# Kernel tuning notes

Hardware: AMD Instinct MI355X
Metric: run time of the kernel (lower is better)

The kernel has to match this reference:

```python
import jax, jax.numpy as jnp
import numpy as np

B, S, DM, H = 4, 4096, 1024, 16
HD = DM // H

def setup_inputs() -> dict:
    key = jax.random.key(0)
    ks = jax.random.split(key, 9)
    sc = 1.0 / np.sqrt(DM)
    return {
        "x": jax.random.normal(ks[0], (B, S, DM), dtype=jnp.float32),
        "Wq": jax.random.normal(ks[1], (DM, DM), dtype=jnp.float32) * sc,
        "bq": jnp.zeros((DM,), dtype=jnp.float32),
        "Wk": jax.random.normal(ks[2], (DM, DM), dtype=jnp.float32) * sc,
        "bk": jnp.zeros((DM,), dtype=jnp.float32),
        "Wv": jax.random.normal(ks[3], (DM, DM), dtype=jnp.float32) * sc,
        "bv": jnp.zeros((DM,), dtype=jnp.float32),
        "Wo": jax.random.normal(ks[4], (DM, DM), dtype=jnp.float32) * sc,
        "bo": jnp.zeros((DM,), dtype=jnp.float32),
    }

def _heads(t):
    # [B,S,DM] -> [B,H,S,HD]
    return t.reshape(B, S, H, HD).transpose(0, 2, 1, 3)

def reference(x, Wq, bq, Wk, bk, Wv, bv, Wo, bo):
    q = _heads(x @ Wq.T + bq)
    k = _heads(x @ Wk.T + bk)
    v = _heads(x @ Wv.T + bv)
    q = jax.nn.elu(q) + 1.0  # positive feature map
    k = jax.nn.elu(k) + 1.0
    # kv aggregation: [B,H,HD,HD]
    kv = jnp.einsum('bhsd,bhse->bhde', k, v)
    qkv = jnp.einsum('bhsd,bhde->bhse', q, kv)  # [B,H,S,HD]
    k_sum = k.sum(axis=2)  # [B,H,HD]
    normalizer = jnp.einsum('bhsd,bhd->bhs', q, k_sum) + 1e-6
    out = qkv / normalizer[..., None]
    out = out.transpose(0, 2, 1, 3).reshape(B, S, DM)
    return out @ Wo.T + bo  # dropout is identity in eval
```

## Files before the change

### kernel.cpp

```cpp
#include <hip/hip_runtime.h>
#include <math.h>

#define NROWS  16384
#define DMODEL 1024
#define NHEAD  16
#define HDIM   64
#define SEQ    4096
#define NBATCH 4
#define NBH    64
#define SCHUNK 16
#define M1     1048576u

typedef __attribute__((ext_vector_type(8))) short bf16x8;
typedef __attribute__((ext_vector_type(4))) float f32x4;

#define VMCNT(N) asm volatile("s_waitcnt vmcnt(" #N ")" ::: "memory")
#define BAR() do { asm volatile("" ::: "memory"); __builtin_amdgcn_s_barrier(); \
                   asm volatile("" ::: "memory"); } while (0)

__device__ __forceinline__ unsigned short f2bf(float f) {
    unsigned u = __float_as_uint(f);
    u += 0x7FFFu + ((u >> 16) & 1u);
    return (unsigned short)(u >> 16);
}
__device__ __forceinline__ float bf2f(unsigned short h) {
    return __uint_as_float((unsigned)h << 16);
}

__device__ __forceinline__ void gload16(const void* g, void* l) {
    __builtin_amdgcn_global_load_lds(
        (const __attribute__((address_space(1))) unsigned int*)g,
        (__attribute__((address_space(3))) unsigned int*)l, 16, 0, 0);
}

__global__ __launch_bounds__(256)
void split_pair(const float* __restrict__ a, unsigned short* __restrict__ hi,
                unsigned short* __restrict__ lo, int n4)
{
    int i = blockIdx.x * 256 + threadIdx.x;
    const int stride = gridDim.x * 256;
    for (; i < n4; i += stride) {
        const float4 v = ((const float4*)a)[i];
        ushort4 H, L;
        H.x = f2bf(v.x); L.x = f2bf(v.x - bf2f(H.x));
        H.y = f2bf(v.y); L.y = f2bf(v.y - bf2f(H.y));
        H.z = f2bf(v.z); L.z = f2bf(v.z - bf2f(H.z));
        H.w = f2bf(v.w); L.w = f2bf(v.w - bf2f(H.w));
        ((ushort4*)hi)[i] = H;
        ((ushort4*)lo)[i] = L;
    }
}

__global__ __launch_bounds__(256)
void split_w4(const float* __restrict__ a0, const float* __restrict__ a1,
              const float* __restrict__ a2, const float* __restrict__ a3,
              unsigned short* __restrict__ hib, unsigned short* __restrict__ lob)
{
    const int y = blockIdx.y;
    const float* src = (y == 0) ? a0 : (y == 1) ? a1 : (y == 2) ? a2 : a3;
    const int i = blockIdx.x * 256 + threadIdx.x;
    const float4 v = ((const float4*)src)[i];
    ushort4 H, L;
    H.x = f2bf(v.x); L.x = f2bf(v.x - bf2f(H.x));
    H.y = f2bf(v.y); L.y = f2bf(v.y - bf2f(H.y));
    H.z = f2bf(v.z); L.z = f2bf(v.z - bf2f(H.z));
    H.w = f2bf(v.w); L.w = f2bf(v.w - bf2f(H.w));
    const size_t o = (size_t)y * M1 + (size_t)i * 4;
    *(ushort4*)&hib[o] = H;
    *(ushort4*)&lob[o] = L;
}

template<int MODE>
__global__ __launch_bounds__(512)
void gemm_t3(const unsigned short* __restrict__ Ah, const unsigned short* __restrict__ Al,
             const unsigned short* __restrict__ WhB, const unsigned short* __restrict__ WlB,
             const float* __restrict__ bias0, const float* __restrict__ bias1,
             float* __restrict__ C0, float* __restrict__ C1, int nbs, int wrow0)
{
    __shared__ unsigned short lds[73728];
    const int t    = threadIdx.x;
    const int lane = t & 63;
    const int wv   = t >> 6;
    const int wr   = wv >> 1;
    const int wcn  = wv & 1;

    const int bid  = blockIdx.x;
    const int swz  = (bid & 7) * ((int)gridDim.x >> 3) + (bid >> 3);
    const int NBm  = (1 << nbs) - 1;
    const int mb   = swz >> nbs;
    const int nb   = swz & NBm;
    const int am0  = mb * 256;
    const int bn0g = wrow0 + nb * 128;

    const int fr   = lane & 15;
    const int j0   = lane >> 4;
    const unsigned fro = (unsigned)((j0 * 16 + fr) * 8);
    const int srcr = lane & 15;
    const int srcc = (lane >> 4) * 8;

    f32x4 acc[4][4];
#pragma unroll
    for (int i = 0; i < 4; ++i)
#pragma unroll
        for (int j = 0; j < 4; ++j)
#pragma unroll
            for (int e = 0; e < 4; ++e) acc[i][j][e] = 0.f;

    auto stage_full = [&](int kt, unsigned wb) {
#pragma unroll
        for (int c = 0; c < 2; ++c) {
            const int ch = wv * 2 + c;
            const size_t ga = (size_t)(am0 + ch * 16 + srcr) * DMODEL + kt * 32 + srcc;
            gload16(Ah + ga, (unsigned short*)&lds[wb + (unsigned)ch * 512u]);
            gload16(Al + ga, (unsigned short*)&lds[wb + 8192u + (unsigned)ch * 512u]);
        }
        const size_t gb = (size_t)(bn0g + wv * 16 + srcr) * DMODEL + kt * 32 + srcc;
        gload16(WhB + gb, (unsigned short*)&lds[wb + 16384u + (unsigned)wv * 512u]);
        gload16(WlB + gb, (unsigned short*)&lds[wb + 20480u + (unsigned)wv * 512u]);
    };

    auto phases = [&](unsigned rd, unsigned wb, int k2, bool doStage) {
        bf16x8 bh[4], bl[4];
#pragma unroll
        for (int j = 0; j < 4; ++j) {
            const unsigned ch = (unsigned)(wcn * 4 + j) * 512u;
            bh[j] = *(const bf16x8*)&lds[rd + 16384u + ch + fro];
            bl[j] = *(const bf16x8*)&lds[rd + 20480u + ch + fro];
        }
#pragma unroll
        for (int p = 0; p < 4; ++p) {
            const unsigned ch = (unsigned)(wr * 4 + p) * 512u;
            const bf16x8 a_h = *(const bf16x8*)&lds[rd + ch + fro];
            const bf16x8 a_l = *(const bf16x8*)&lds[rd + 8192u + ch + fro];
            if (doStage) {
                if (p < 2) {
                    const int cch = wv * 2 + p;
                    const size_t ga = (size_t)(am0 + cch * 16 + srcr) * DMODEL + k2 * 32 + srcc;
                    gload16(Ah + ga, (unsigned short*)&lds[wb + (unsigned)cch * 512u]);
                    gload16(Al + ga, (unsigned short*)&lds[wb + 8192u + (unsigned)cch * 512u]);
                } else if (p == 2) {
                    const size_t gb = (size_t)(bn0g + wv * 16 + srcr) * DMODEL + k2 * 32 + srcc;
                    gload16(WhB + gb, (unsigned short*)&lds[wb + 16384u + (unsigned)wv * 512u]);
                    gload16(WlB + gb, (unsigned short*)&lds[wb + 20480u + (unsigned)wv * 512u]);
                }
            }
            __builtin_amdgcn_s_setprio(1);
#pragma unroll
            for (int j = 0; j < 4; ++j) {
                acc[p][j] = __builtin_amdgcn_mfma_f32_16x16x32_bf16(a_h, bh[j], acc[p][j], 0, 0, 0);
                acc[p][j] = __builtin_amdgcn_mfma_f32_16x16x32_bf16(a_h, bl[j], acc[p][j], 0, 0, 0);
                acc[p][j] = __builtin_amdgcn_mfma_f32_16x16x32_bf16(a_l, bh[j], acc[p][j], 0, 0, 0);
            }
            __builtin_amdgcn_s_setprio(0);
        }
    };

    stage_full(0, 0u);
    stage_full(1, 24576u);

    for (int kt = 0; kt < 30; kt += 3) {
        VMCNT(6); BAR(); phases(0u,     49152u, kt + 2, true);
        VMCNT(6); BAR(); phases(24576u, 0u,     kt + 3, true);
        VMCNT(6); BAR(); phases(49152u, 24576u, kt + 4, true);
    }
    VMCNT(6); BAR(); phases(0u,     0u, 0, false);
    VMCNT(0); BAR(); phases(24576u, 0u, 0, false);

    const bool elu = (MODE == 1) || (MODE == 2 && nb < 8);
    float* Cm = C0;
    const float* bm = bias0;
    int coff = 0;
    if (MODE == 2 && nb >= 8) { Cm = C1; bm = bias1; coff = 1024; }
    const int crow0 = am0 + wr * 64 + (lane >> 4) * 4;
    const int ccol0 = nb * 128 + wcn * 64 + fr - coff;
#pragma unroll
    for (int j = 0; j < 4; ++j) {
        const int col = ccol0 + j * 16;
        const float bv = bm[col];
#pragma unroll
        for (int i = 0; i < 4; ++i) {
            const int row = crow0 + i * 16;
#pragma unroll
            for (int r = 0; r < 4; ++r) {
                float v = acc[i][j][r] + bv;
                if (elu) v = (v > 0.f) ? (v + 1.f) : __expf(v);
                Cm[(size_t)(row + r) * DMODEL + col] = v;
            }
        }
    }
}

__global__ __launch_bounds__(512)
void kv_partial(const float* __restrict__ k, const float* __restrict__ v,
                float* __restrict__ kvp, float* __restrict__ ksp)
{
    __shared__ float Ks[32][64];
    __shared__ float Vs[32][64];
    const int t  = threadIdx.x;
    const int bh = blockIdx.x;
    const int b  = bh >> 4;
    const int h  = bh & 15;
    const int sc = blockIdx.y;
    const int d  = t & 63;
    const int e0 = (t >> 6) * 8;

    float acc[8];
#pragma unroll
    for (int j = 0; j < 8; ++j) acc[j] = 0.f;
    float ks = 0.f;

    const size_t rowbase = (size_t)b * SEQ;
    const int sbeg = sc * (SEQ / SCHUNK);
    const int send = sbeg + (SEQ / SCHUNK);
    const int lrow = t >> 4;
    const int lc4  = (t & 15) * 4;

    for (int s0 = sbeg; s0 < send; s0 += 32) {
        const size_t g = (rowbase + s0 + lrow) * DMODEL + h * HDIM + lc4;
        *(float4*)&Ks[lrow][lc4] = *(const float4*)&k[g];
        *(float4*)&Vs[lrow][lc4] = *(const float4*)&v[g];
        __syncthreads();
#pragma unroll 8
        for (int sp = 0; sp < 32; ++sp) {
            const float kd = Ks[sp][d];
            if (t < 64) ks += Ks[sp][t];
            const float4 v0 = *(const float4*)&Vs[sp][e0 + 0];
            const float4 v1 = *(const float4*)&Vs[sp][e0 + 4];
            acc[0] = fmaf(kd, v0.x, acc[0]);  acc[1] = fmaf(kd, v0.y, acc[1]);
            acc[2] = fmaf(kd, v0.z, acc[2]);  acc[3] = fmaf(kd, v0.w, acc[3]);
            acc[4] = fmaf(kd, v1.x, acc[4]);  acc[5] = fmaf(kd, v1.y, acc[5]);
            acc[6] = fmaf(kd, v1.z, acc[6]);  acc[7] = fmaf(kd, v1.w, acc[7]);
        }
        __syncthreads();
    }

    const size_t base = ((size_t)sc * NBH + bh) * HDIM;
    float4 o0; o0.x = acc[0]; o0.y = acc[1]; o0.z = acc[2]; o0.w = acc[3];
    float4 o1; o1.x = acc[4]; o1.y = acc[5]; o1.z = acc[6]; o1.w = acc[7];
    *(float4*)&kvp[(base + d) * HDIM + e0 + 0] = o0;
    *(float4*)&kvp[(base + d) * HDIM + e0 + 4] = o1;
    if (t < 64) ksp[base + t] = ks;
}

__global__ __launch_bounds__(256)
void kv_reduce(const float* __restrict__ kvp, const float* __restrict__ ksp,
               float* __restrict__ kv, float* __restrict__ ksum)
{
    const int i = blockIdx.x * 256 + threadIdx.x;
    const int NKV = NBH * HDIM * HDIM;
    if (i < NKV) {
        float s = 0.f;
#pragma unroll
        for (int c = 0; c < SCHUNK; ++c) s += kvp[(size_t)c * NKV + i];
        kv[i] = s;
    }
    if (i < NBH * HDIM) {
        float s = 0.f;
#pragma unroll
        for (int c = 0; c < SCHUNK; ++c) s += ksp[(size_t)c * NBH * HDIM + i];
        ksum[i] = s;
    }
}

__global__ __launch_bounds__(256)
void qkv_norm(const float* __restrict__ q, const float* __restrict__ kv,
              const float* __restrict__ ksum,
              unsigned short* __restrict__ ah, unsigned short* __restrict__ al)
{
    __shared__ float Qs[64][68];
    __shared__ float KVs[64][64];
    __shared__ float kss[64];
    const int t  = threadIdx.x;
    const int s0 = blockIdx.x * 64;
    const int b  = blockIdx.y;
    const int h  = blockIdx.z;
    const int bh = b * NHEAD + h;

#pragma unroll
    for (int i = 0; i < 4; ++i) {
        const int idx = i * 256 + t;
        const int row = idx >> 4;
        const int c4  = (idx & 15) * 4;
        const float4 vq = *(const float4*)&q[((size_t)b * SEQ + s0 + row) * DMODEL + h * HDIM + c4];
        *(float4*)&Qs[row][c4] = vq;
        *(float4*)&((float*)KVs)[idx * 4] = *(const float4*)&kv[(size_t)bh * HDIM * HDIM + idx * 4];
    }
    if (t < 64) kss[t] = ksum[(size_t)bh * HDIM + t];
    __syncthreads();

    const int r  = t >> 2;
    const int e0 = (t & 3) * 16;
    float out[16];
#pragma unroll
    for (int j = 0; j < 16; ++j) out[j] = 0.f;
    float nrm = 0.f;

#pragma unroll 8
    for (int d = 0; d < 64; ++d) {
        const float qd = Qs[r][d];
        nrm = fmaf(qd, kss[d], nrm);
        const float4 k0 = *(const float4*)&KVs[d][e0 + 0];
        const float4 k1 = *(const float4*)&KVs[d][e0 + 4];
        const float4 k2 = *(const float4*)&KVs[d][e0 + 8];
        const float4 k3 = *(const float4*)&KVs[d][e0 + 12];
        out[0]  = fmaf(qd, k0.x, out[0]);  out[1]  = fmaf(qd, k0.y, out[1]);
        out[2]  = fmaf(qd, k0.z, out[2]);  out[3]  = fmaf(qd, k0.w, out[3]);
        out[4]  = fmaf(qd, k1.x, out[4]);  out[5]  = fmaf(qd, k1.y, out[5]);
        out[6]  = fmaf(qd, k1.z, out[6]);  out[7]  = fmaf(qd, k1.w, out[7]);
        out[8]  = fmaf(qd, k2.x, out[8]);  out[9]  = fmaf(qd, k2.y, out[9]);
        out[10] = fmaf(qd, k2.z, out[10]); out[11] = fmaf(qd, k2.w, out[11]);
        out[12] = fmaf(qd, k3.x, out[12]); out[13] = fmaf(qd, k3.y, out[13]);
        out[14] = fmaf(qd, k3.z, out[14]); out[15] = fmaf(qd, k3.w, out[15]);
    }

    const float inv = 1.f / (nrm + 1e-6f);
    const size_t gbase = ((size_t)b * SEQ + s0 + r) * DMODEL + h * HDIM + e0;
#pragma unroll
    for (int g4 = 0; g4 < 4; ++g4) {
        ushort4 H, L;
        const float v0 = out[g4*4+0] * inv;
        const float v1 = out[g4*4+1] * inv;
        const float v2 = out[g4*4+2] * inv;
        const float v3 = out[g4*4+3] * inv;
        H.x = f2bf(v0); L.x = f2bf(v0 - bf2f(H.x));
        H.y = f2bf(v1); L.y = f2bf(v1 - bf2f(H.y));
        H.z = f2bf(v2); L.z = f2bf(v2 - bf2f(H.z));
        H.w = f2bf(v3); L.w = f2bf(v3 - bf2f(H.w));
        *(ushort4*)&ah[gbase + g4 * 4] = H;
        *(ushort4*)&al[gbase + g4 * 4] = L;
    }
}

extern "C" void kernel_launch(void* const* d_in, const int* in_sizes, int n_in,
                              void* d_out, int out_size, void* d_ws, size_t ws_size,
                              hipStream_t stream)
{
    const float* x  = (const float*)d_in[0];
    const float* Wq = (const float*)d_in[1];
    const float* bq = (const float*)d_in[2];
    const float* Wk = (const float*)d_in[3];
    const float* bk = (const float*)d_in[4];
    const float* Wv = (const float*)d_in[5];
    const float* bv = (const float*)d_in[6];
    const float* Wo = (const float*)d_in[7];
    const float* bo = (const float*)d_in[8];

    unsigned short* xh  = (unsigned short*)d_ws;
    unsigned short* xl  = xh + (size_t)NROWS * DMODEL;
    unsigned short* hib = xl + (size_t)NROWS * DMODEL;
    unsigned short* lob = hib + 4u * M1;
    float* buf0 = (float*)(lob + 4u * M1);
    float* kv   = buf0 + (size_t)NROWS * DMODEL;
    float* ksum = kv + NBH * HDIM * HDIM;
    float* kvp  = ksum + NBH * HDIM;
    float* ksp  = kvp + (size_t)SCHUNK * NBH * HDIM * HDIM;
    float* vbuf = (float*)d_out;

    const int n4x = NROWS * DMODEL / 4;

    split_w4<<<dim3(1024, 4), 256, 0, stream>>>(Wq, Wk, Wv, Wo, hib, lob);
    split_pair<<<4096, 256, 0, stream>>>(x, xh, xl, n4x);
    gemm_t3<2><<<1024, 512, 0, stream>>>(xh, xl, hib, lob, bk, bv, buf0, vbuf, 4, 1024);
    kv_partial<<<dim3(NBH, SCHUNK), 512, 0, stream>>>(buf0, vbuf, kvp, ksp);
    kv_reduce<<<1024, 256, 0, stream>>>(kvp, ksp, kv, ksum);
    gemm_t3<1><<<512, 512, 0, stream>>>(xh, xl, hib, lob, bq, nullptr, buf0, nullptr, 3, 0);
    qkv_norm<<<dim3(SEQ / 64, NBATCH, NHEAD), 256, 0, stream>>>(buf0, kv, ksum, xh, xl);
    gemm_t3<0><<<512, 512, 0, stream>>>(xh, xl, hib, lob, bo, nullptr, (float*)d_out, nullptr, 3, 3072);
}
```

Measured before the change: 551.2 us.

## Rewrite split-bf16 GEMM with 32x32 MFMA and 256x256 tiles

Replaces the 256x128 tile GEMM built on 16x16x32 MFMAs with a 256x256 tile GEMM built on 32x32x16 MFMAs. Each step covers K=16, and the kernel double-buffers A and W in 64KB of LDS with staggered staging of A and W inside the iteration. Weight order is rearranged to K,V,Q,O so that each GEMM can address its weights with a plain pointer offset. The larger tile and larger MFMA are meant to raise arithmetic intensity and cut LDS traffic per flop, at the cost of fewer blocks, shallower prefetch and more barriers per K-step.

```diff
diff --git a/kernel.cpp b/kernel.cpp
--- a/kernel.cpp
+++ b/kernel.cpp
@@ -11,8 +11,9 @@
 #define SCHUNK 16
 #define M1     1048576u
 
-typedef __attribute__((ext_vector_type(8))) short bf16x8;
-typedef __attribute__((ext_vector_type(4))) float f32x4;
+typedef __attribute__((ext_vector_type(8)))  short bf16x8;
+typedef __attribute__((ext_vector_type(4)))  float f32x4;
+typedef __attribute__((ext_vector_type(16))) float f32x16;
 
 #define VMCNT(N) asm volatile("s_waitcnt vmcnt(" #N ")" ::: "memory")
 #define BAR() do { asm volatile("" ::: "memory"); __builtin_amdgcn_s_barrier(); \
@@ -72,119 +73,126 @@
 
 template<int MODE>
 __global__ __launch_bounds__(512)
-void gemm_t3(const unsigned short* __restrict__ Ah, const unsigned short* __restrict__ Al,
-             const unsigned short* __restrict__ WhB, const unsigned short* __restrict__ WlB,
-             const float* __restrict__ bias0, const float* __restrict__ bias1,
-             float* __restrict__ C0, float* __restrict__ C1, int nbs, int wrow0)
-{
-    __shared__ unsigned short lds[73728];
+void gemm32(const unsigned short* __restrict__ Ah, const unsigned short* __restrict__ Al,
+            const unsigned short* __restrict__ Wh, const unsigned short* __restrict__ Wl,
+            const float* __restrict__ bias0, const float* __restrict__ bias1,
+            float* __restrict__ C0, float* __restrict__ C1, int nbs)
+{
+    __shared__ unsigned short lds[32768];
     const int t    = threadIdx.x;
     const int lane = t & 63;
     const int wv   = t >> 6;
-    const int wr   = wv >> 1;
-    const int wcn  = wv & 1;
-
-    const int bid  = blockIdx.x;
-    const int swz  = (bid & 7) * ((int)gridDim.x >> 3) + (bid >> 3);
-    const int NBm  = (1 << nbs) - 1;
-    const int mb   = swz >> nbs;
-    const int nb   = swz & NBm;
-    const int am0  = mb * 256;
-    const int bn0g = wrow0 + nb * 128;
-
-    const int fr   = lane & 15;
-    const int j0   = lane >> 4;
-    const unsigned fro = (unsigned)((j0 * 16 + fr) * 8);
-    const int srcr = lane & 15;
-    const int srcc = (lane >> 4) * 8;
-
-    f32x4 acc[4][4];
+    const int wr   = wv >> 2;
+    const int wcn  = wv & 3;
+
+    const int bid = blockIdx.x;
+    const int swz = (bid & 7) * ((int)gridDim.x >> 3) + (bid >> 3);
+    const int mb  = swz >> nbs;
+    const int nb  = swz & ((1 << nbs) - 1);
+    const int am0 = mb * 256;
+    const int bn0 = nb * 256;
+
+    const int l31  = lane & 31;
+    const int hi5  = lane >> 5;
+    const unsigned fro = (unsigned)lane * 8u;
+
+    f32x16 acc[4][2];
 #pragma unroll
     for (int i = 0; i < 4; ++i)
 #pragma unroll
-        for (int j = 0; j < 4; ++j)
-#pragma unroll
-            for (int e = 0; e < 4; ++e) acc[i][j][e] = 0.f;
-
-    auto stage_full = [&](int kt, unsigned wb) {
-#pragma unroll
-        for (int c = 0; c < 2; ++c) {
-            const int ch = wv * 2 + c;
-            const size_t ga = (size_t)(am0 + ch * 16 + srcr) * DMODEL + kt * 32 + srcc;
-            gload16(Ah + ga, (unsigned short*)&lds[wb + (unsigned)ch * 512u]);
-            gload16(Al + ga, (unsigned short*)&lds[wb + 8192u + (unsigned)ch * 512u]);
-        }
-        const size_t gb = (size_t)(bn0g + wv * 16 + srcr) * DMODEL + kt * 32 + srcc;
-        gload16(WhB + gb, (unsigned short*)&lds[wb + 16384u + (unsigned)wv * 512u]);
-        gload16(WlB + gb, (unsigned short*)&lds[wb + 20480u + (unsigned)wv * 512u]);
+        for (int j = 0; j < 2; ++j)
+#pragma unroll
+            for (int e = 0; e < 16; ++e) acc[i][j][e] = 0.f;
+
+    auto stageA = [&](int kt) {
+        const unsigned bb = ((unsigned)kt & 1u) * 16384u;
+        const size_t g = (size_t)(am0 + wv * 32 + l31) * DMODEL + kt * 16 + hi5 * 8;
+        gload16(Ah + g, (unsigned short*)&lds[bb + (unsigned)wv * 512u]);
+        gload16(Al + g, (unsigned short*)&lds[bb + 4096u + (unsigned)wv * 512u]);
     };
-
-    auto phases = [&](unsigned rd, unsigned wb, int k2, bool doStage) {
-        bf16x8 bh[4], bl[4];
-#pragma unroll
-        for (int j = 0; j < 4; ++j) {
-            const unsigned ch = (unsigned)(wcn * 4 + j) * 512u;
-            bh[j] = *(const bf16x8*)&lds[rd + 16384u + ch + fro];
-            bl[j] = *(const bf16x8*)&lds[rd + 20480u + ch + fro];
-        }
-#pragma unroll
-        for (int p = 0; p < 4; ++p) {
-            const unsigned ch = (unsigned)(wr * 4 + p) * 512u;
-            const bf16x8 a_h = *(const bf16x8*)&lds[rd + ch + fro];
-            const bf16x8 a_l = *(const bf16x8*)&lds[rd + 8192u + ch + fro];
-            if (doStage) {
-                if (p < 2) {
-                    const int cch = wv * 2 + p;
-                    const size_t ga = (size_t)(am0 + cch * 16 + srcr) * DMODEL + k2 * 32 + srcc;
-                    gload16(Ah + ga, (unsigned short*)&lds[wb + (unsigned)cch * 512u]);
-                    gload16(Al + ga, (unsigned short*)&lds[wb + 8192u + (unsigned)cch * 512u]);
-                } else if (p == 2) {
-                    const size_t gb = (size_t)(bn0g + wv * 16 + srcr) * DMODEL + k2 * 32 + srcc;
-                    gload16(WhB + gb, (unsigned short*)&lds[wb + 16384u + (unsigned)wv * 512u]);
-                    gload16(WlB + gb, (unsigned short*)&lds[wb + 20480u + (unsigned)wv * 512u]);
-                }
+    auto stageW = [&](int kt) {
+        const unsigned bb = ((unsigned)kt & 1u) * 16384u;
+        const size_t g = (size_t)(bn0 + wv * 32 + l31) * DMODEL + kt * 16 + hi5 * 8;
+        gload16(Wh + g, (unsigned short*)&lds[bb + 8192u  + (unsigned)wv * 512u]);
+        gload16(Wl + g, (unsigned short*)&lds[bb + 12288u + (unsigned)wv * 512u]);
+    };
+
+    stageA(0); stageW(0); stageW(1);
+
+#pragma unroll 2
+    for (int kt = 0; kt < 64; ++kt) {
+        if (kt < 63) { VMCNT(2); } else { VMCNT(0); }
+        BAR();
+        const unsigned bb = ((unsigned)kt & 1u) * 16384u;
+
+        bf16x8 bh[2], bl[2];
+#pragma unroll
+        for (int ni = 0; ni < 2; ++ni) {
+            const unsigned ch = (unsigned)(wcn * 2 + ni) * 512u;
+            bh[ni] = *(const bf16x8*)&lds[bb + 8192u  + ch + fro];
+            bl[ni] = *(const bf16x8*)&lds[bb + 12288u + ch + fro];
+        }
+        bf16x8 ah[2], al[2];
+#pragma unroll
+        for (int i2 = 0; i2 < 2; ++i2) {
+            const unsigned ch = (unsigned)(wr * 4 + i2) * 512u;
+            ah[i2] = *(const bf16x8*)&lds[bb + ch + fro];
+            al[i2] = *(const bf16x8*)&lds[bb + 4096u + ch + fro];
+        }
+        if (kt + 1 < 64) stageA(kt + 1);
+        __builtin_amdgcn_s_barrier();
+        __builtin_amdgcn_s_setprio(1);
+#pragma unroll
+        for (int i2 = 0; i2 < 2; ++i2)
+#pragma unroll
+            for (int ni = 0; ni < 2; ++ni) {
+                acc[i2][ni] = __builtin_amdgcn_mfma_f32_32x32x16_bf16(ah[i2], bh[ni], acc[i2][ni], 0, 0, 0);
+                acc[i2][ni] = __builtin_amdgcn_mfma_f32_32x32x16_bf16(ah[i2], bl[ni], acc[i2][ni], 0, 0, 0);
+                acc[i2][ni] = __builtin_amdgcn_mfma_f32_32x32x16_bf16(al[i2], bh[ni], acc[i2][ni], 0, 0, 0);
             }
-            __builtin_amdgcn_s_setprio(1);
-#pragma unroll
-            for (int j = 0; j < 4; ++j) {
-                acc[p][j] = __builtin_amdgcn_mfma_f32_16x16x32_bf16(a_h, bh[j], acc[p][j], 0, 0, 0);
-                acc[p][j] = __builtin_amdgcn_mfma_f32_16x16x32_bf16(a_h, bl[j], acc[p][j], 0, 0, 0);
-                acc[p][j] = __builtin_amdgcn_mfma_f32_16x16x32_bf16(a_l, bh[j], acc[p][j], 0, 0, 0);
+        __builtin_amdgcn_s_setprio(0);
+
+#pragma unroll
+        for (int i2 = 0; i2 < 2; ++i2) {
+            const unsigned ch = (unsigned)(wr * 4 + 2 + i2) * 512u;
+            ah[i2] = *(const bf16x8*)&lds[bb + ch + fro];
+            al[i2] = *(const bf16x8*)&lds[bb + 4096u + ch + fro];
+        }
+        __builtin_amdgcn_s_barrier();
+        if (kt + 2 < 64) stageW(kt + 2);
+        __builtin_amdgcn_s_setprio(1);
+#pragma unroll
+        for (int i2 = 0; i2 < 2; ++i2)
+#pragma unroll
+            for (int ni = 0; ni < 2; ++ni) {
+                acc[2 + i2][ni] = __builtin_amdgcn_mfma_f32_32x32x16_bf16(ah[i2], bh[ni], acc[2 + i2][ni], 0, 0, 0);
+                acc[2 + i2][ni] = __builtin_amdgcn_mfma_f32_32x32x16_bf16(ah[i2], bl[ni], acc[2 + i2][ni], 0, 0, 0);
+                acc[2 + i2][ni] = __builtin_amdgcn_mfma_f32_32x32x16_bf16(al[i2], bh[ni], acc[2 + i2][ni], 0, 0, 0);
             }
-            __builtin_amdgcn_s_setprio(0);
-        }
-    };
-
-    stage_full(0, 0u);
-    stage_full(1, 24576u);
-
-    for (int kt = 0; kt < 30; kt += 3) {
-        VMCNT(6); BAR(); phases(0u,     49152u, kt + 2, true);
-        VMCNT(6); BAR(); phases(24576u, 0u,     kt + 3, true);
-        VMCNT(6); BAR(); phases(49152u, 24576u, kt + 4, true);
-    }
-    VMCNT(6); BAR(); phases(0u,     0u, 0, false);
-    VMCNT(0); BAR(); phases(24576u, 0u, 0, false);
-
-    const bool elu = (MODE == 1) || (MODE == 2 && nb < 8);
+        __builtin_amdgcn_s_setprio(0);
+    }
+
+    bool elu = (MODE == 1);
     float* Cm = C0;
     const float* bm = bias0;
-    int coff = 0;
-    if (MODE == 2 && nb >= 8) { Cm = C1; bm = bias1; coff = 1024; }
-    const int crow0 = am0 + wr * 64 + (lane >> 4) * 4;
-    const int ccol0 = nb * 128 + wcn * 64 + fr - coff;
-#pragma unroll
-    for (int j = 0; j < 4; ++j) {
-        const int col = ccol0 + j * 16;
+    int colb = bn0;
+    if (MODE == 2) {
+        if (nb < 4) { elu = true; }
+        else        { Cm = C1; bm = bias1; colb = (nb - 4) * 256; }
+    }
+    const int crow00 = am0 + wr * 128 + 4 * hi5;
+#pragma unroll
+    for (int ni = 0; ni < 2; ++ni) {
+        const int col = colb + wcn * 64 + ni * 32 + l31;
         const float bv = bm[col];
 #pragma unroll
-        for (int i = 0; i < 4; ++i) {
-            const int row = crow0 + i * 16;
-#pragma unroll
-            for (int r = 0; r < 4; ++r) {
-                float v = acc[i][j][r] + bv;
+        for (int mi = 0; mi < 4; ++mi) {
+#pragma unroll
+            for (int r = 0; r < 16; ++r) {
+                const int row = crow00 + mi * 32 + (r & 3) + 8 * (r >> 2);
+                float v = acc[mi][ni][r] + bv;
                 if (elu) v = (v > 0.f) ? (v + 1.f) : __expf(v);
-                Cm[(size_t)(row + r) * DMODEL + col] = v;
+                Cm[(size_t)row * DMODEL + col] = v;
             }
         }
     }
@@ -347,9 +355,9 @@
 
     unsigned short* xh  = (unsigned short*)d_ws;
     unsigned short* xl  = xh + (size_t)NROWS * DMODEL;
-    unsigned short* hib = xl + (size_t)NROWS * DMODEL;
-    unsigned short* lob = hib + 4u * M1;
-    float* buf0 = (float*)(lob + 4u * M1);
+    unsigned short* whi = xl + (size_t)NROWS * DMODEL;
+    unsigned short* wlo = whi + 4u * M1;
+    float* buf0 = (float*)(wlo + 4u * M1);
     float* kv   = buf0 + (size_t)NROWS * DMODEL;
     float* ksum = kv + NBH * HDIM * HDIM;
     float* kvp  = ksum + NBH * HDIM;
@@ -358,12 +366,14 @@
 
     const int n4x = NROWS * DMODEL / 4;
 
-    split_w4<<<dim3(1024, 4), 256, 0, stream>>>(Wq, Wk, Wv, Wo, hib, lob);
+    split_w4<<<dim3(1024, 4), 256, 0, stream>>>(Wk, Wv, Wq, Wo, whi, wlo);
     split_pair<<<4096, 256, 0, stream>>>(x, xh, xl, n4x);
-    gemm_t3<2><<<1024, 512, 0, stream>>>(xh, xl, hib, lob, bk, bv, buf0, vbuf, 4, 1024);
+    gemm32<2><<<512, 512, 0, stream>>>(xh, xl, whi, wlo, bk, bv, buf0, vbuf, 3);
     kv_partial<<<dim3(NBH, SCHUNK), 512, 0, stream>>>(buf0, vbuf, kvp, ksp);
     kv_reduce<<<1024, 256, 0, stream>>>(kvp, ksp, kv, ksum);
-    gemm_t3<1><<<512, 512, 0, stream>>>(xh, xl, hib, lob, bq, nullptr, buf0, nullptr, 3, 0);
+    gemm32<1><<<256, 512, 0, stream>>>(xh, xl, whi + 2u * M1, wlo + 2u * M1,
+                                       bq, nullptr, buf0, nullptr, 2);
     qkv_norm<<<dim3(SEQ / 64, NBATCH, NHEAD), 256, 0, stream>>>(buf0, kv, ksum, xh, xl);
-    gemm_t3<0><<<512, 512, 0, stream>>>(xh, xl, hib, lob, bo, nullptr, (float*)d_out, nullptr, 3, 3072);
-}
+    gemm32<0><<<256, 512, 0, stream>>>(xh, xl, whi + 3u * M1, wlo + 3u * M1,
+                                       bo, nullptr, (float*)d_out, nullptr, 2);
+}
```

New measurement: 536.7 us. 2.6% less time.
